# Optimization experiments

Hardware: AMD Instinct MI355X
Metric: run time of the kernel (lower is better)

Reference implementation:

```python
import jax, jax.numpy as jnp
import numpy as np

N, E, F_IN, H, L, E_FEAT, G, OUT = 100000, 1600000, 8, 128, 4, 16, 256, 256


def setup_inputs() -> dict:
    key = jax.random.key(0)
    ks = jax.random.split(key, 12)
    inp = {
        "x": jax.random.normal(ks[0], (N, F_IN), jnp.float32),
        "edge_index": jax.random.randint(ks[1], (2, E), 0, N),
        "edge_attr": jax.random.uniform(ks[2], (E, E_FEAT), jnp.float32),
        "batch": jnp.sort(jax.random.randint(ks[3], (N,), 0, G)),
        "emb_W": jax.random.normal(ks[4], (F_IN, H), jnp.float32) / np.sqrt(F_IN),
        "emb_b": jnp.zeros((H,), jnp.float32),
        "edge_W": jax.random.normal(ks[5], (L, E_FEAT, H), jnp.float32) / np.sqrt(E_FEAT),
        "edge_b": jnp.zeros((L, H), jnp.float32),
        "nn_W": jax.random.normal(ks[6], (L, H, H), jnp.float32) / np.sqrt(H),
        "nn_b": jnp.zeros((L, H), jnp.float32),
        "bn_g": jnp.ones((L, H), jnp.float32),
        "bn_b": jnp.zeros((L, H), jnp.float32),
        "lin_W": jax.random.normal(ks[7], (H, OUT), jnp.float32) / np.sqrt(H),
        "lin_b": jnp.zeros((OUT,), jnp.float32),
    }
    return inp


def reference(x, edge_index, edge_attr, batch, emb_W, emb_b, edge_W, edge_b,
              nn_W, nn_b, bn_g, bn_b, lin_W, lin_b):
    eps_bn = 1e-5
    src, dst = edge_index[0], edge_index[1]
    h = x @ emb_W + emb_b  # node embedding [N,H]
    for l in range(L):
        e = edge_attr @ edge_W[l] + edge_b[l]          # [E,H] edge embedding
        msg = jax.nn.relu(h[src] + e)                   # gather + message
        agg = jax.ops.segment_sum(msg, dst, num_segments=N)  # scatter-add
        hc = (h + agg) @ nn_W[l] + nn_b[l]             # GINE nn (eps=0)
        mu = jnp.mean(hc, axis=0)
        var = jnp.mean((hc - mu) ** 2, axis=0)          # biased var (train BN)
        hc = (hc - mu) * jax.lax.rsqrt(var + eps_bn) * bn_g[l] + bn_b[l]
        hc = jax.nn.gelu(hc, approximate=False)
        h = h + hc                                      # 'res' residual
    out = h @ lin_W + lin_b                             # [N,OUT]
    rep = jax.ops.segment_sum(out, batch, num_segments=G)  # global_add_pool
    return rep
```

## Files before the change

kernel.cpp:

```cpp
#include <hip/hip_runtime.h>
#include <hip/hip_fp16.h>
#include <math.h>

#define GG 256

typedef __attribute__((ext_vector_type(8))) short short8;
typedef __attribute__((ext_vector_type(4))) float f32x4;
typedef _Float16 half4v __attribute__((ext_vector_type(4)));
typedef __attribute__((ext_vector_type(8))) unsigned uint8v;

__device__ __forceinline__ unsigned short f2bf(float x) {
  union { float f; unsigned u; } v; v.f = x;
  unsigned r = v.u + 0x7fff + ((v.u >> 16) & 1);
  return (unsigned short)(r >> 16);
}

__device__ __forceinline__ unsigned pack_h2(float a, float b) {
  __half2 h = __floats2half2_rn(a, b);
  return *(unsigned*)&h;
}

__device__ __forceinline__ uint8v sload8(const void* p) {
  uint8v r;
  asm volatile("s_load_dwordx8 %0, %1, 0x0"
               : "=s"(r) : "s"((unsigned long long)p));
  return r;
}
__device__ __forceinline__ void swait() {
  asm volatile("s_waitcnt lgkmcnt(0)" ::: "memory");
  __builtin_amdgcn_sched_barrier(0);
}
__device__ __forceinline__ void swait2(uint8v& a, uint8v& b) {
  asm volatile("s_waitcnt lgkmcnt(0)" : "+s"(a), "+s"(b) :: "memory");
  __builtin_amdgcn_sched_barrier(0);
}

__global__ __launch_bounds__(256) void k_emb(const float* __restrict__ x,
    const float* __restrict__ W, const float* __restrict__ b,
    float* __restrict__ h, unsigned short* __restrict__ hb, int N) {
  int idx = blockIdx.x * 256 + threadIdx.x;
  if (idx >= N * 32) return;
  int n = idx >> 5, q = idx & 31;
  const float* xr = x + (size_t)n * 8;
  float xs[8];
#pragma unroll
  for (int k = 0; k < 8; ++k) xs[k] = xr[k];
  float4 acc = ((const float4*)b)[q];
#pragma unroll
  for (int k = 0; k < 8; ++k) {
    float4 w = ((const float4*)(W + (size_t)k * 128))[q];
    acc.x += xs[k] * w.x; acc.y += xs[k] * w.y;
    acc.z += xs[k] * w.z; acc.w += xs[k] * w.w;
  }
  ((float4*)h)[idx] = acc;
  ushort4 hv4 = make_ushort4(f2bf(acc.x), f2bf(acc.y), f2bf(acc.z), f2bf(acc.w));
  *(ushort4*)(hb + (size_t)idx * 4) = hv4;
}

__global__ __launch_bounds__(256) void k_wconv2(const float* __restrict__ eW,
    unsigned* __restrict__ eWf) {
  int i = blockIdx.x * 256 + threadIdx.x;
  if (i >= 2048) return;
  int lane = i & 63, nt = (i >> 6) & 7, l = i >> 9;
  int l15 = lane & 15, quad = lane >> 4;
  const float* base = eW + (size_t)l * 16 * 128 + (size_t)(nt * 16 + l15);
  unsigned lo = pack_h2(base[(quad * 4 + 0) * 128], base[(quad * 4 + 1) * 128]);
  unsigned hi = pack_h2(base[(quad * 4 + 2) * 128], base[(quad * 4 + 3) * 128]);
  eWf[(size_t)i * 2] = lo;
  eWf[(size_t)i * 2 + 1] = hi;
}

__global__ __launch_bounds__(256) void k_nnconv(const float* __restrict__ W,
    unsigned short* __restrict__ WT) {
  int i = blockIdx.x * 256 + threadIdx.x;
  if (i >= 4 * 128 * 128) return;
  int n = i & 127, k = (i >> 7) & 127, l = i >> 14;
  WT[((size_t)(l * 128 + n)) * 128 + k] = f2bf(W[i]);
}

__global__ void k_hist(const int* __restrict__ dst, int* __restrict__ deg, int E) {
  int e = blockIdx.x * blockDim.x + threadIdx.x;
  if (e < E) atomicAdd(&deg[dst[e]], 1);
}

__global__ __launch_bounds__(256) void k_scan_reduce(const int* __restrict__ deg,
    int* __restrict__ bsum, int N) {
  __shared__ int sd[256];
  int i = blockIdx.x * 256 + threadIdx.x;
  sd[threadIdx.x] = (i < N) ? deg[i] : 0;
  __syncthreads();
  for (int s = 128; s > 0; s >>= 1) {
    if (threadIdx.x < s) sd[threadIdx.x] += sd[threadIdx.x + s];
    __syncthreads();
  }
  if (threadIdx.x == 0) bsum[blockIdx.x] = sd[0];
}

__global__ __launch_bounds__(512) void k_scan_mid(int* bsum, int nb) {
  __shared__ int sd[512];
  int t = threadIdx.x;
  int v = (t < nb) ? bsum[t] : 0;
  sd[t] = v; __syncthreads();
  for (int d = 1; d < 512; d <<= 1) {
    int xv = (t >= d) ? sd[t - d] : 0;
    __syncthreads();
    sd[t] += xv;
    __syncthreads();
  }
  if (t < nb) bsum[t] = sd[t] - v;
}

__global__ __launch_bounds__(256) void k_scan_final(const int* __restrict__ deg,
    const int* __restrict__ bsum, int* __restrict__ offs,
    int* __restrict__ cursor, int N) {
  __shared__ int sd[256];
  int t = threadIdx.x;
  int i = blockIdx.x * 256 + t;
  int v = (i < N) ? deg[i] : 0;
  sd[t] = v; __syncthreads();
  for (int d = 1; d < 256; d <<= 1) {
    int xv = (t >= d) ? sd[t - d] : 0;
    __syncthreads();
    sd[t] += xv;
    __syncthreads();
  }
  int off = bsum[blockIdx.x] + sd[t] - v;
  if (i < N) {
    offs[i] = off; cursor[i] = off;
    if (i == N - 1) offs[N] = off + v;
  }
}

__global__ void k_fill(const int* __restrict__ src, const int* __restrict__ dst,
    const float* __restrict__ attr, int* __restrict__ cursor,
    int* __restrict__ csrc, uint4* __restrict__ cattr16, int E) {
  int e = blockIdx.x * blockDim.x + threadIdx.x;
  if (e >= E) return;
  int d = dst[e];
  int pos = atomicAdd(&cursor[d], 1);
  csrc[pos] = src[e];
  const float4* a = (const float4*)(attr + (size_t)e * 16);
  float4 a0 = a[0], a1 = a[1], a2 = a[2], a3 = a[3];
  uint4 o0, o1;
  o0.x = pack_h2(a0.x, a0.y); o0.y = pack_h2(a0.z, a0.w);
  o0.z = pack_h2(a1.x, a1.y); o0.w = pack_h2(a1.z, a1.w);
  o1.x = pack_h2(a2.x, a2.y); o1.y = pack_h2(a2.z, a2.w);
  o1.z = pack_h2(a3.x, a3.y); o1.w = pack_h2(a3.z, a3.w);
  cattr16[(size_t)pos * 2] = o0;
  cattr16[(size_t)pos * 2 + 1] = o1;
}

__global__ void k_gstart(const int* __restrict__ batch, int* __restrict__ gstart,
                         int N, int Gn) {
  int i = blockIdx.x * blockDim.x + threadIdx.x;
  if (i >= N) return;
  int b = batch[i];
  if (i == 0) { for (int g = 0; g <= b; ++g) gstart[g] = 0; }
  else { int bp = batch[i - 1]; for (int g = bp + 1; g <= b; ++g) gstart[g] = i; }
  if (i == N - 1) { for (int g = b + 1; g <= Gn; ++g) gstart[g] = N; }
}

__global__ __launch_bounds__(256) void k_edge_agg(const float* __restrict__ h,
    const unsigned* __restrict__ hb32,
    const uint4* __restrict__ cattr16, const int* __restrict__ csrc,
    const int* __restrict__ offs, const unsigned* __restrict__ eWf,
    const float* __restrict__ eb, unsigned* __restrict__ hpa16,
    float* __restrict__ cstats, int N) {
  __shared__ __half elds_all[4][16 * 136];
  int t = threadIdx.x;
  if (blockIdx.x == 0) cstats[t] = 0.f;
  int lane = t & 63;
  int l15 = lane & 15, quad = lane >> 4;
  int wid = blockIdx.x * 4 + (t >> 6);
  int nw = gridDim.x * 4;
  __half* elds = elds_all[t >> 6];
  uint2 bfr[8];
#pragma unroll
  for (int nt = 0; nt < 8; ++nt) bfr[nt] = ((const uint2*)eWf)[nt * 64 + lane];
  float2 bias = *(const float2*)(eb + 2 * lane);
  const unsigned* hb_l = hb32 + lane;

#define GI(r, SC)                                                           \
  unsigned u##r = 0;                                                        \
  if (j0 + (r) < je) u##r = hb_l[(size_t)(unsigned)(SC) * 64];

#define EPI(r, UU, AX, AY)                                                  \
  if (j0 + (r) < je) {                                                      \
    __half2 ev2 = *(__half2*)&elds[(r) * 136 + 2 * lane];                   \
    union { unsigned uu; float ff; } c0, c1;                                \
    c0.uu = (UU) << 16; c1.uu = (UU) & 0xffff0000u;                         \
    AX += fmaxf(__low2float(ev2) + bias.x + c0.ff, 0.f);                    \
    AY += fmaxf(__high2float(ev2) + bias.y + c1.ff, 0.f);                   \
  }

#define LOADA(DST, J0)                                                      \
  DST = *(const uint2*)((const char*)cattr16 +                              \
        ((size_t)(unsigned)((J0) + l15)) * 32 + quad * 8);

  for (int n = wid; n < N; n += nw) {
    int jb = __builtin_amdgcn_readfirstlane(offs[n]);
    int je = __builtin_amdgcn_readfirstlane(offs[n + 1]);
    float ax = 0.f, ay = 0.f, bx = 0.f, by = 0.f;
    if (jb < je) {
      uint8v scA = sload8((const char*)csrc + ((size_t)(unsigned)jb << 2));
      uint8v scB = sload8((const char*)csrc + ((size_t)(unsigned)(jb + 8) << 2));
      uint2 araw;
      LOADA(araw, jb)
      swait2(scA, scB);
      for (int j0 = jb;;) {
        GI(0, scA[0]) GI(1, scA[1]) GI(2, scA[2]) GI(3, scA[3])
        GI(4, scA[4]) GI(5, scA[5]) GI(6, scA[6]) GI(7, scA[7])
        GI(8, scB[0]) GI(9, scB[1]) GI(10, scB[2]) GI(11, scB[3])
        GI(12, scB[4]) GI(13, scB[5]) GI(14, scB[6]) GI(15, scB[7])
        bool more = (j0 + 16 < je);
        uint8v scA2, scB2;
        uint2 araw2;
        if (more) {
          scA2 = sload8((const char*)csrc + ((size_t)(unsigned)(j0 + 16) << 2));
          scB2 = sload8((const char*)csrc + ((size_t)(unsigned)(j0 + 24) << 2));
          LOADA(araw2, j0 + 16)
        }
        half4v av;
        __builtin_memcpy(&av, &araw, 8);
        f32x4 ee[8];
#pragma unroll
        for (int nt = 0; nt < 8; ++nt) {
          half4v bv;
          __builtin_memcpy(&bv, &bfr[nt], 8);
          ee[nt] = __builtin_amdgcn_mfma_f32_16x16x16f16(
              av, bv, (f32x4){0.f, 0.f, 0.f, 0.f}, 0, 0, 0);
        }
#pragma unroll
        for (int nt = 0; nt < 8; ++nt)
#pragma unroll
          for (int reg = 0; reg < 4; ++reg)
            elds[(quad * 4 + reg) * 136 + nt * 16 + l15] =
                __float2half(ee[nt][reg]);
        EPI(0, u0, ax, ay)  EPI(1, u1, bx, by)
        EPI(2, u2, ax, ay)  EPI(3, u3, bx, by)
        EPI(4, u4, ax, ay)  EPI(5, u5, bx, by)
        EPI(6, u6, ax, ay)  EPI(7, u7, bx, by)
        EPI(8, u8, ax, ay)  EPI(9, u9, bx, by)
        EPI(10, u10, ax, ay) EPI(11, u11, bx, by)
        EPI(12, u12, ax, ay) EPI(13, u13, bx, by)
        EPI(14, u14, ax, ay) EPI(15, u15, bx, by)
        j0 += 16;
        if (!more) break;
        swait2(scA2, scB2);
        scA = scA2; scB = scB2; araw = araw2;
      }
    }
    float2 hvv = *(const float2*)(h + (size_t)n * 128 + 2 * lane);
    float rx = hvv.x + ax + bx;
    float ry = hvv.y + ay + by;
    hpa16[(size_t)n * 64 + lane] = ((unsigned)f2bf(ry) << 16) | (unsigned)f2bf(rx);
  }
#undef GI
#undef EPI
#undef LOADA
}

__global__ __launch_bounds__(256) void k_gemm_mfma(
    const unsigned short* __restrict__ A16, const unsigned short* __restrict__ WT16,
    const float* __restrict__ bias, float* __restrict__ hc,
    float* __restrict__ cstats, int N) {
  __shared__ short a_lds[128 * 136];
  __shared__ short w_lds[128 * 136];
  int t = threadIdx.x;
  int rowbase = blockIdx.x * 128;
  {
    int r = t >> 1;
    int off = (t & 1) * 64;
    const short* ga = (const short*)A16 + (size_t)(rowbase + r) * 128 + off;
    short* la = &a_lds[r * 136 + off];
    const short* gw = (const short*)WT16 + (size_t)r * 128 + off;
    short* lw = &w_lds[r * 136 + off];
    if (rowbase + r < N) {
#pragma unroll
      for (int jj = 0; jj < 8; ++jj)
        *(uint4*)(la + jj * 8) = *(const uint4*)(ga + jj * 8);
    } else {
#pragma unroll
      for (int jj = 0; jj < 8; ++jj)
        *(uint4*)(la + jj * 8) = make_uint4(0, 0, 0, 0);
    }
#pragma unroll
    for (int jj = 0; jj < 8; ++jj)
      *(uint4*)(lw + jj * 8) = *(const uint4*)(gw + jj * 8);
  }
  __syncthreads();
  int w = t >> 6;
  int lane = t & 63;
  int l15 = lane & 15, quad = lane >> 4;
  f32x4 acc[2][8];
#pragma unroll
  for (int rt = 0; rt < 2; ++rt)
#pragma unroll
    for (int nt = 0; nt < 8; ++nt)
      acc[rt][nt] = (f32x4){0.f, 0.f, 0.f, 0.f};
#pragma unroll
  for (int kc = 0; kc < 4; ++kc) {
    int k0 = kc * 32 + quad * 8;
    short8 af0 = *(const short8*)&a_lds[(w * 32 + l15) * 136 + k0];
    short8 af1 = *(const short8*)&a_lds[(w * 32 + 16 + l15) * 136 + k0];
#pragma unroll
    for (int nt = 0; nt < 8; ++nt) {
      short8 bf = *(const short8*)&w_lds[(nt * 16 + l15) * 136 + k0];
      acc[0][nt] = __builtin_amdgcn_mfma_f32_16x16x32_bf16(af0, bf, acc[0][nt], 0, 0, 0);
      acc[1][nt] = __builtin_amdgcn_mfma_f32_16x16x32_bf16(af1, bf, acc[1][nt], 0, 0, 0);
    }
  }
  float sA[8], sQ[8];
#pragma unroll
  for (int nt = 0; nt < 8; ++nt) { sA[nt] = 0.f; sQ[nt] = 0.f; }
#pragma unroll
  for (int nt = 0; nt < 8; ++nt) {
    int col = nt * 16 + l15;
    float bv = bias[col];
#pragma unroll
    for (int rt = 0; rt < 2; ++rt) {
      int rbase = rowbase + w * 32 + rt * 16 + quad * 4;
#pragma unroll
      for (int reg = 0; reg < 4; ++reg) {
        int row = rbase + reg;
        float v = acc[rt][nt][reg] + bv;
        if (row < N) {
          hc[(size_t)row * 128 + col] = v;
          sA[nt] += v; sQ[nt] += v * v;
        }
      }
    }
  }
#pragma unroll
  for (int nt = 0; nt < 8; ++nt) {
    sA[nt] += __shfl_xor(sA[nt], 16);
    sA[nt] += __shfl_xor(sA[nt], 32);
    sQ[nt] += __shfl_xor(sQ[nt], 16);
    sQ[nt] += __shfl_xor(sQ[nt], 32);
  }
  __syncthreads();
  float* sdA = (float*)a_lds;
  float* sdQ = (float*)w_lds;
  if (quad == 0) {
#pragma unroll
    for (int nt = 0; nt < 8; ++nt) {
      sdA[w * 128 + nt * 16 + l15] = sA[nt];
      sdQ[w * 128 + nt * 16 + l15] = sQ[nt];
    }
  }
  __syncthreads();
  if (t < 128) {
    float s = sdA[t] + sdA[128 + t] + sdA[256 + t] + sdA[384 + t];
    float s2 = sdQ[t] + sdQ[128 + t] + sdQ[256 + t] + sdQ[384 + t];
    atomicAdd(&cstats[t], s);
    atomicAdd(&cstats[128 + t], s2);
  }
}

__global__ __launch_bounds__(256) void k_bn(const float* __restrict__ hc,
    const float* __restrict__ cstats,
    const float* __restrict__ g, const float* __restrict__ bb,
    float* __restrict__ h, unsigned short* __restrict__ hb, int N) {
  int idx = blockIdx.x * 256 + threadIdx.x;
  if (idx >= N * 32) return;
  int q = idx & 31;
  float invN = 1.f / (float)N;
  float4 cs = ((const float4*)cstats)[q];
  float4 cq = ((const float4*)cstats)[q + 32];
  float4 gv = ((const float4*)g)[q];
  float4 bv = ((const float4*)bb)[q];
  float4 v = ((const float4*)hc)[idx];
  float4 hv = ((const float4*)h)[idx];
#define BN1(X)                                                      \
  { float mu = cs.X * invN;                                         \
    float var = cq.X * invN - mu * mu;                              \
    float xn = (v.X - mu) * rsqrtf(var + 1e-5f) * gv.X + bv.X;      \
    hv.X += 0.5f * xn * (1.f + erff(xn * 0.70710678118654752f)); }
  BN1(x) BN1(y) BN1(z) BN1(w)
#undef BN1
  ((float4*)h)[idx] = hv;
  if (hb) {
    ushort4 hv4 = make_ushort4(f2bf(hv.x), f2bf(hv.y), f2bf(hv.z), f2bf(hv.w));
    *(ushort4*)(hb + (size_t)idx * 4) = hv4;
  }
}

__global__ __launch_bounds__(256) void k_poolfinal(const float* __restrict__ h,
    const int* __restrict__ gstart, const float* __restrict__ W,
    const float* __restrict__ b, float* __restrict__ out) {
  int g = blockIdx.x;
  int t = threadIdx.x, c = t & 127, half = t >> 7;
  int n0 = gstart[g], n1 = gstart[g + 1];
  float s = 0.f;
  for (int n = n0 + half; n < n1; n += 2) s += h[(size_t)n * 128 + c];
  __shared__ float ls[256];
  __shared__ float pr[128];
  ls[t] = s; __syncthreads();
  if (t < 128) pr[t] = ls[t] + ls[t + 128];
  __syncthreads();
  float cnt = (float)(n1 - n0);
  float acc = cnt * b[t];
#pragma unroll 8
  for (int k = 0; k < 128; ++k) acc += pr[k] * W[(size_t)k * 256 + t];
  out[(size_t)g * 256 + t] = acc;
}

extern "C" void kernel_launch(void* const* d_in, const int* in_sizes, int n_in,
                              void* d_out, int out_size, void* d_ws, size_t ws_size,
                              hipStream_t stream) {
  const float* x     = (const float*)d_in[0];
  const int*   eidx  = (const int*)d_in[1];
  const float* eattr = (const float*)d_in[2];
  const int*   batch = (const int*)d_in[3];
  const float* embW  = (const float*)d_in[4];
  const float* embB  = (const float*)d_in[5];
  const float* edgeW = (const float*)d_in[6];
  const float* edgeB = (const float*)d_in[7];
  const float* nnW   = (const float*)d_in[8];
  const float* nnB   = (const float*)d_in[9];
  const float* bnG   = (const float*)d_in[10];
  const float* bnB   = (const float*)d_in[11];
  const float* linW  = (const float*)d_in[12];
  const float* linB  = (const float*)d_in[13];
  float* out = (float*)d_out;

  int N = in_sizes[0] / 8;
  int E = in_sizes[1] / 2;
  const int* src = eidx;
  const int* dst = eidx + E;

  char* wptr = (char*)d_ws;
  auto alloc = [&](size_t bytes) {
    char* p = wptr; wptr += (bytes + 255) & ~(size_t)255; return p;
  };
  float* h      = (float*)alloc((size_t)N * 128 * 4);
  float* hc     = (float*)alloc((size_t)N * 128 * 4);
  unsigned short* hb = (unsigned short*)alloc((size_t)N * 128 * 2);
  unsigned* hpa16 = (unsigned*)alloc((size_t)N * 64 * 4);
  uint4* cattr16 = (uint4*)alloc((size_t)E * 32 + 1024);
  int*   csrc   = (int*)alloc((size_t)E * 4 + 256);
  int*   offs   = (int*)alloc((size_t)(N + 1) * 4);
  int*   cursor = (int*)alloc((size_t)N * 4);
  int*   deg    = (int*)alloc((size_t)N * 4);
  int nb = (N + 255) / 256;
  int*   bsum   = (int*)alloc((size_t)nb * 4);
  float* cstats = (float*)alloc(256 * 4);
  unsigned* eWf = (unsigned*)alloc(4096 * 4);
  unsigned short* WT16 = (unsigned short*)alloc(4 * 128 * 128 * 2);
  int*   gstart = (int*)alloc((size_t)(GG + 1) * 4);

  int q32 = (N * 32 + 255) / 256;

  hipMemsetAsync(deg, 0, (size_t)N * 4, stream);
  k_emb<<<q32, 256, 0, stream>>>(x, embW, embB, h, hb, N);
  k_wconv2<<<8, 256, 0, stream>>>(edgeW, eWf);
  k_nnconv<<<256, 256, 0, stream>>>(nnW, WT16);
  k_hist<<<(E + 255) / 256, 256, 0, stream>>>(dst, deg, E);
  k_scan_reduce<<<nb, 256, 0, stream>>>(deg, bsum, N);
  k_scan_mid<<<1, 512, 0, stream>>>(bsum, nb);
  k_scan_final<<<nb, 256, 0, stream>>>(deg, bsum, offs, cursor, N);
  k_fill<<<(E + 255) / 256, 256, 0, stream>>>(src, dst, eattr, cursor, csrc, cattr16, E);
  k_gstart<<<(N + 255) / 256, 256, 0, stream>>>(batch, gstart, N, GG);

  int gblk = (N + 127) / 128;
  for (int l = 0; l < 4; ++l) {
    k_edge_agg<<<8192, 256, 0, stream>>>(h, (const unsigned*)hb, cattr16, csrc,
        offs, eWf + (size_t)l * 1024, edgeB + (size_t)l * 128, hpa16, cstats, N);
    k_gemm_mfma<<<gblk, 256, 0, stream>>>((const unsigned short*)hpa16,
        WT16 + (size_t)l * 128 * 128, nnB + (size_t)l * 128, hc, cstats, N);
    k_bn<<<q32, 256, 0, stream>>>(hc, cstats,
        bnG + (size_t)l * 128, bnB + (size_t)l * 128, h, (l == 3) ? nullptr : hb, N);
  }
  k_poolfinal<<<GG, 256, 0, stream>>>(h, gstart, linW, linB, out);
}
```

Measured before the change: 1.028 ms.

## Compute BN stats from input covariance and fuse BatchNorm into GEMM epilogue

The batch-norm mean and variance of hc = A·W + b are now computed analytically from A's column sums and the Gram matrix AᵀA. A new MFMA covariance kernel builds these, and a small double-precision kernel turns them into per-channel mean and rstd. This lets the GEMM apply BN, GELU and the residual update directly in its epilogue, removing the hc write/read round trip and the separate BN kernel. In exchange it adds an extra full pass over hpa16, a 128x128 atomic reduction and a memset per layer. The variance is formed as E[x²]-mu² from bf16 inputs, which carries some risk of cancellation.

```diff
diff --git a/kernel.cpp b/kernel.cpp
--- a/kernel.cpp
+++ b/kernel.cpp
@@ -25,10 +25,6 @@
   asm volatile("s_load_dwordx8 %0, %1, 0x0"
                : "=s"(r) : "s"((unsigned long long)p));
   return r;
-}
-__device__ __forceinline__ void swait() {
-  asm volatile("s_waitcnt lgkmcnt(0)" ::: "memory");
-  __builtin_amdgcn_sched_barrier(0);
 }
 __device__ __forceinline__ void swait2(uint8v& a, uint8v& b) {
   asm volatile("s_waitcnt lgkmcnt(0)" : "+s"(a), "+s"(b) :: "memory");
@@ -164,11 +160,9 @@
     const unsigned* __restrict__ hb32,
     const uint4* __restrict__ cattr16, const int* __restrict__ csrc,
     const int* __restrict__ offs, const unsigned* __restrict__ eWf,
-    const float* __restrict__ eb, unsigned* __restrict__ hpa16,
-    float* __restrict__ cstats, int N) {
+    const float* __restrict__ eb, unsigned* __restrict__ hpa16, int N) {
   __shared__ __half elds_all[4][16 * 136];
   int t = threadIdx.x;
-  if (blockIdx.x == 0) cstats[t] = 0.f;
   int lane = t & 63;
   int l15 = lane & 15, quad = lane >> 4;
   int wid = blockIdx.x * 4 + (t >> 6);
@@ -260,12 +254,127 @@
 #undef LOADA
 }
 
+__global__ __launch_bounds__(256) void k_cov(const uint4* __restrict__ hpa4,
+    float* __restrict__ S, float* __restrict__ csum, int N) {
+  __shared__ __align__(16) short tile[32 * 140];
+  __shared__ float scr[128 * 33];
+  int t = threadIdx.x;
+  int lane = t & 63, w = t >> 6;
+  int l15 = lane & 15, quad = lane >> 4;
+  int nl = t >> 3, seg = t & 7;
+  int chunk = (((N + 127) / 128) + 31) & ~31;
+  int base = blockIdx.x * chunk;
+  int nsteps = chunk / 32;
+  float cs[16];
+#pragma unroll
+  for (int i = 0; i < 16; ++i) cs[i] = 0.f;
+  f32x4 acc[2][8];
+#pragma unroll
+  for (int i = 0; i < 2; ++i)
+#pragma unroll
+    for (int j = 0; j < 8; ++j) acc[i][j] = (f32x4){0.f, 0.f, 0.f, 0.f};
+  int w2 = w * 2;
+  for (int ks = 0; ks < nsteps; ++ks) {
+    int node = base + ks * 32 + nl;
+    uint4 a = make_uint4(0, 0, 0, 0), b = make_uint4(0, 0, 0, 0);
+    if (node < N) {
+      a = hpa4[(size_t)node * 16 + seg * 2];
+      b = hpa4[(size_t)node * 16 + seg * 2 + 1];
+    }
+    __syncthreads();
+    *(uint2*)&tile[nl * 140 + seg * 16]      = make_uint2(a.x, a.y);
+    *(uint2*)&tile[nl * 140 + seg * 16 + 4]  = make_uint2(a.z, a.w);
+    *(uint2*)&tile[nl * 140 + seg * 16 + 8]  = make_uint2(b.x, b.y);
+    *(uint2*)&tile[nl * 140 + seg * 16 + 12] = make_uint2(b.z, b.w);
+    unsigned uu[8] = {a.x, a.y, a.z, a.w, b.x, b.y, b.z, b.w};
+#pragma unroll
+    for (int k = 0; k < 8; ++k) {
+      union { unsigned u; float f; } lo, hi;
+      lo.u = uu[k] << 16; hi.u = uu[k] & 0xffff0000u;
+      cs[2 * k] += lo.f; cs[2 * k + 1] += hi.f;
+    }
+    __syncthreads();
+    short8 fb[8];
+#pragma unroll
+    for (int g = 0; g < 8; ++g)
+#pragma unroll
+      for (int e = 0; e < 8; ++e)
+        fb[g][e] = tile[(quad * 8 + e) * 140 + g * 16 + l15];
+    short8 fa0, fa1;
+#pragma unroll
+    for (int e = 0; e < 8; ++e) {
+      fa0[e] = tile[(quad * 8 + e) * 140 + w2 * 16 + l15];
+      fa1[e] = tile[(quad * 8 + e) * 140 + (w2 + 1) * 16 + l15];
+    }
+#pragma unroll
+    for (int j = 0; j < 8; ++j) {
+      acc[0][j] = __builtin_amdgcn_mfma_f32_16x16x32_bf16(fa0, fb[j], acc[0][j], 0, 0, 0);
+      acc[1][j] = __builtin_amdgcn_mfma_f32_16x16x32_bf16(fa1, fb[j], acc[1][j], 0, 0, 0);
+    }
+  }
+#pragma unroll
+  for (int i = 0; i < 2; ++i)
+#pragma unroll
+    for (int j = 0; j < 8; ++j)
+#pragma unroll
+      for (int reg = 0; reg < 4; ++reg) {
+        int row = (w2 + i) * 16 + quad * 4 + reg;
+        atomicAdd(&S[(size_t)row * 128 + j * 16 + l15], acc[i][j][reg]);
+      }
+  __syncthreads();
+#pragma unroll
+  for (int f = 0; f < 16; ++f) scr[(seg * 16 + f) * 33 + nl] = cs[f];
+  __syncthreads();
+  if (t < 128) {
+    float s = 0.f;
+#pragma unroll 8
+    for (int k = 0; k < 32; ++k) s += scr[t * 33 + k];
+    atomicAdd(&csum[t], s);
+  }
+}
+
+__global__ __launch_bounds__(128) void k_stats(const float* __restrict__ S,
+    const float* __restrict__ csum, const unsigned short* __restrict__ WT,
+    const float* __restrict__ bias, float* __restrict__ must,
+    float* __restrict__ rstds, int N) {
+  __shared__ float wv[128];
+  __shared__ double red[128];
+  __shared__ double red2[128];
+  int c = blockIdx.x, r = threadIdx.x;
+  union { unsigned u; float f; } wc;
+  wc.u = (unsigned)WT[(size_t)c * 128 + r] << 16;
+  wv[r] = wc.f;
+  __syncthreads();
+  const float* Sr = S + (size_t)r * 128;
+  double dr = 0.0;
+#pragma unroll 8
+  for (int k = 0; k < 128; ++k) dr += (double)Sr[k] * (double)wv[k];
+  red[r] = dr * (double)wv[r];
+  red2[r] = (double)csum[r] * (double)wv[r];
+  __syncthreads();
+  for (int s = 64; s > 0; s >>= 1) {
+    if (r < s) { red[r] += red[r + s]; red2[r] += red2[r + s]; }
+    __syncthreads();
+  }
+  if (r == 0) {
+    double invN = 1.0 / (double)N;
+    double m0 = red2[0] * invN;
+    double var = red[0] * invN - m0 * m0;
+    if (var < 0.0) var = 0.0;
+    must[c] = (float)(m0 + (double)bias[c]);
+    rstds[c] = (float)(1.0 / sqrt(var + 1e-5));
+  }
+}
+
 __global__ __launch_bounds__(256) void k_gemm_mfma(
     const unsigned short* __restrict__ A16, const unsigned short* __restrict__ WT16,
-    const float* __restrict__ bias, float* __restrict__ hc,
-    float* __restrict__ cstats, int N) {
-  __shared__ short a_lds[128 * 136];
-  __shared__ short w_lds[128 * 136];
+    const float* __restrict__ bias, const float* __restrict__ must,
+    const float* __restrict__ rstds, const float* __restrict__ g,
+    const float* __restrict__ bb, float* __restrict__ h,
+    unsigned short* __restrict__ hb, int N) {
+  __shared__ __align__(16) char smem[69632];
+  short* a_lds = (short*)smem;
+  short* w_lds = (short*)(smem + 34816);
   int t = threadIdx.x;
   int rowbase = blockIdx.x * 128;
   {
@@ -310,78 +419,44 @@
       acc[1][nt] = __builtin_amdgcn_mfma_f32_16x16x32_bf16(af1, bf, acc[1][nt], 0, 0, 0);
     }
   }
-  float sA[8], sQ[8];
-#pragma unroll
-  for (int nt = 0; nt < 8; ++nt) { sA[nt] = 0.f; sQ[nt] = 0.f; }
+  __syncthreads();
+  float* fb = (float*)smem;
 #pragma unroll
   for (int nt = 0; nt < 8; ++nt) {
     int col = nt * 16 + l15;
     float bv = bias[col];
 #pragma unroll
     for (int rt = 0; rt < 2; ++rt) {
-      int rbase = rowbase + w * 32 + rt * 16 + quad * 4;
-#pragma unroll
-      for (int reg = 0; reg < 4; ++reg) {
-        int row = rbase + reg;
-        float v = acc[rt][nt][reg] + bv;
-        if (row < N) {
-          hc[(size_t)row * 128 + col] = v;
-          sA[nt] += v; sQ[nt] += v * v;
-        }
-      }
-    }
-  }
-#pragma unroll
-  for (int nt = 0; nt < 8; ++nt) {
-    sA[nt] += __shfl_xor(sA[nt], 16);
-    sA[nt] += __shfl_xor(sA[nt], 32);
-    sQ[nt] += __shfl_xor(sQ[nt], 16);
-    sQ[nt] += __shfl_xor(sQ[nt], 32);
-  }
-  __syncthreads();
-  float* sdA = (float*)a_lds;
-  float* sdQ = (float*)w_lds;
-  if (quad == 0) {
-#pragma unroll
-    for (int nt = 0; nt < 8; ++nt) {
-      sdA[w * 128 + nt * 16 + l15] = sA[nt];
-      sdQ[w * 128 + nt * 16 + l15] = sQ[nt];
-    }
-  }
-  __syncthreads();
-  if (t < 128) {
-    float s = sdA[t] + sdA[128 + t] + sdA[256 + t] + sdA[384 + t];
-    float s2 = sdQ[t] + sdQ[128 + t] + sdQ[256 + t] + sdQ[384 + t];
-    atomicAdd(&cstats[t], s);
-    atomicAdd(&cstats[128 + t], s2);
-  }
-}
-
-__global__ __launch_bounds__(256) void k_bn(const float* __restrict__ hc,
-    const float* __restrict__ cstats,
-    const float* __restrict__ g, const float* __restrict__ bb,
-    float* __restrict__ h, unsigned short* __restrict__ hb, int N) {
-  int idx = blockIdx.x * 256 + threadIdx.x;
-  if (idx >= N * 32) return;
-  int q = idx & 31;
-  float invN = 1.f / (float)N;
-  float4 cs = ((const float4*)cstats)[q];
-  float4 cq = ((const float4*)cstats)[q + 32];
-  float4 gv = ((const float4*)g)[q];
-  float4 bv = ((const float4*)bb)[q];
-  float4 v = ((const float4*)hc)[idx];
-  float4 hv = ((const float4*)h)[idx];
-#define BN1(X)                                                      \
-  { float mu = cs.X * invN;                                         \
-    float var = cq.X * invN - mu * mu;                              \
-    float xn = (v.X - mu) * rsqrtf(var + 1e-5f) * gv.X + bv.X;      \
-    hv.X += 0.5f * xn * (1.f + erff(xn * 0.70710678118654752f)); }
-  BN1(x) BN1(y) BN1(z) BN1(w)
+      int rl = w * 32 + rt * 16 + quad * 4;
+#pragma unroll
+      for (int reg = 0; reg < 4; ++reg)
+        fb[(rl + reg) * 132 + col] = acc[rt][nt][reg] + bv;
+    }
+  }
+  __syncthreads();
+  int r2 = t >> 1, halfp = t & 1;
+  int grow = rowbase + r2;
+  if (grow < N) {
+    float4* hrow = (float4*)(h + (size_t)grow * 128);
+    ushort4* hbrow = hb ? (ushort4*)(hb + (size_t)grow * 128) : (ushort4*)0;
+#pragma unroll 4
+    for (int i = 0; i < 16; ++i) {
+      int c4 = halfp * 16 + i;
+      float4 v = *(float4*)&fb[r2 * 132 + c4 * 4];
+      float4 m4 = ((const float4*)must)[c4];
+      float4 s4 = ((const float4*)rstds)[c4];
+      float4 g4 = ((const float4*)g)[c4];
+      float4 b4 = ((const float4*)bb)[c4];
+      float4 hv = hrow[c4];
+#define BN1(X)                                                       \
+      { float xn = (v.X - m4.X) * s4.X * g4.X + b4.X;                \
+        hv.X += 0.5f * xn * (1.f + erff(xn * 0.70710678118654752f)); }
+      BN1(x) BN1(y) BN1(z) BN1(w)
 #undef BN1
-  ((float4*)h)[idx] = hv;
-  if (hb) {
-    ushort4 hv4 = make_ushort4(f2bf(hv.x), f2bf(hv.y), f2bf(hv.z), f2bf(hv.w));
-    *(ushort4*)(hb + (size_t)idx * 4) = hv4;
+      hrow[c4] = hv;
+      if (hbrow)
+        hbrow[c4] = make_ushort4(f2bf(hv.x), f2bf(hv.y), f2bf(hv.z), f2bf(hv.w));
+    }
   }
 }
 
@@ -434,7 +509,6 @@
     char* p = wptr; wptr += (bytes + 255) & ~(size_t)255; return p;
   };
   float* h      = (float*)alloc((size_t)N * 128 * 4);
-  float* hc     = (float*)alloc((size_t)N * 128 * 4);
   unsigned short* hb = (unsigned short*)alloc((size_t)N * 128 * 2);
   unsigned* hpa16 = (unsigned*)alloc((size_t)N * 64 * 4);
   uint4* cattr16 = (uint4*)alloc((size_t)E * 32 + 1024);
@@ -444,7 +518,10 @@
   int*   deg    = (int*)alloc((size_t)N * 4);
   int nb = (N + 255) / 256;
   int*   bsum   = (int*)alloc((size_t)nb * 4);
-  float* cstats = (float*)alloc(256 * 4);
+  float* S      = (float*)alloc(128 * 128 * 4);
+  float* csum   = (float*)alloc(128 * 4);
+  float* must   = (float*)alloc(128 * 4);
+  float* rstds  = (float*)alloc(128 * 4);
   unsigned* eWf = (unsigned*)alloc(4096 * 4);
   unsigned short* WT16 = (unsigned short*)alloc(4 * 128 * 128 * 2);
   int*   gstart = (int*)alloc((size_t)(GG + 1) * 4);
@@ -464,12 +541,16 @@
 
   int gblk = (N + 127) / 128;
   for (int l = 0; l < 4; ++l) {
+    hipMemsetAsync(S, 0, 128 * 128 * 4 + 512, stream);
     k_edge_agg<<<8192, 256, 0, stream>>>(h, (const unsigned*)hb, cattr16, csrc,
-        offs, eWf + (size_t)l * 1024, edgeB + (size_t)l * 128, hpa16, cstats, N);
+        offs, eWf + (size_t)l * 1024, edgeB + (size_t)l * 128, hpa16, N);
+    k_cov<<<128, 256, 0, stream>>>((const uint4*)hpa16, S, csum, N);
+    k_stats<<<128, 128, 0, stream>>>(S, csum, WT16 + (size_t)l * 128 * 128,
+        nnB + (size_t)l * 128, must, rstds, N);
     k_gemm_mfma<<<gblk, 256, 0, stream>>>((const unsigned short*)hpa16,
-        WT16 + (size_t)l * 128 * 128, nnB + (size_t)l * 128, hc, cstats, N);
-    k_bn<<<q32, 256, 0, stream>>>(hc, cstats,
-        bnG + (size_t)l * 128, bnB + (size_t)l * 128, h, (l == 3) ? nullptr : hb, N);
+        WT16 + (size_t)l * 128 * 128, nnB + (size_t)l * 128, must, rstds,
+        bnG + (size_t)l * 128, bnB + (size_t)l * 128, h,
+        (l == 3) ? (unsigned short*)0 : hb, N);
   }
   k_poolfinal<<<GG, 256, 0, stream>>>(h, gstart, linW, linB, out);
 }
```

Result: slower. 1.332 ms (+29.6%).
